# Kernel optimization log

Measured on AMD Instinct MI355X. Metric: run time of the kernel, lower is better.

The kernel has to match this reference:

```python
import jax, jax.numpy as jnp
import numpy as np

B, S, D, H = 2, 2048, 1024, 16
DH = D // H  # 64
SCALE = DH ** -0.5


def setup_inputs() -> dict:
    key = jax.random.key(0)
    ks = jax.random.split(key, 6)
    std = D ** -0.5
    return {
        "Q": jax.random.normal(ks[0], (B, S, D), jnp.float32),
        "prev": jax.random.normal(ks[1], (B, H, S, S), jnp.float32),
        "W_qkv": jax.random.normal(ks[2], (D, 3 * D), jnp.float32) * std,
        "b_qkv": jax.random.normal(ks[3], (3 * D,), jnp.float32) * 0.01,
        "W_out": jax.random.normal(ks[4], (D, D), jnp.float32) * std,
        "b_out": jax.random.normal(ks[5], (D,), jnp.float32) * 0.01,
    }


def reference(Q, prev, W_qkv, b_qkv, W_out, b_out):
    # fused QKV projection: [B,S,3D]
    qkv = jnp.einsum("bsd,de->bse", Q, W_qkv) + b_qkv
    # [B,S,H,3*DH] then split into q,k,v each [B,S,H,DH]
    qkv = qkv.reshape(B, S, H, 3 * DH)
    q, k, v = jnp.split(qkv, 3, axis=-1)
    # scores [B,H,S,S] with residual attention add
    scores = jnp.einsum("bqhd,bkhd->bhqk", q, k) * SCALE + prev
    attn = jax.nn.softmax(scores, axis=-1)  # dropout p=0.0 -> identity
    # context [B,S,H,DH] -> [B,S,D]
    context = jnp.einsum("bhqk,bkhd->bqhd", attn, v).reshape(B, S, D)
    output = jnp.einsum("bsd,de->bse", context, W_out) + b_out
    return output, scores
```

## Files before the change

kernel.cpp:

```cpp
#include <hip/hip_runtime.h>

typedef __attribute__((ext_vector_type(8))) short bf16x8;
typedef __attribute__((ext_vector_type(4))) float f32x4;
typedef __attribute__((ext_vector_type(4))) unsigned short u16x4;
typedef unsigned short ushort_t;
typedef unsigned int uint32;

constexpr int B_ = 2, S_ = 2048, D_ = 1024, H_ = 16, DH_ = 64;
constexpr int M_TOK = B_ * S_;
constexpr int N_QKV = 3 * D_;

#define DEV __device__ __forceinline__

DEV ushort_t f2bf(float f) {
  uint32 u = __builtin_bit_cast(uint32, f);
  u += 0x7fffu + ((u >> 16) & 1u);
  return (ushort_t)(u >> 16);
}

DEV void gll16(const void* g, void* l) {
  __builtin_amdgcn_global_load_lds(
      (const __attribute__((address_space(1))) void*)g,
      (__attribute__((address_space(3))) void*)l, 16, 0, 0);
}

__global__ __launch_bounds__(256) void k_cvt_q(const float* __restrict__ in,
                                               ushort_t* __restrict__ out) {
  int i = (blockIdx.x * 256 + threadIdx.x) * 4;
  float4 v = *(const float4*)(in + i);
  u16x4 o;
  o.x = f2bf(v.x); o.y = f2bf(v.y); o.z = f2bf(v.z); o.w = f2bf(v.w);
  *(u16x4*)(out + i) = o;
}

__global__ __launch_bounds__(256) void k_transpose_cvt(const float* __restrict__ in,
                                                       ushort_t* __restrict__ out,
                                                       int R, int C) {
  __shared__ float t[32][33];
  int bx = blockIdx.x, by = blockIdx.y;
  int tx = threadIdx.x & 31, ty = threadIdx.x >> 5;
#pragma unroll
  for (int i = 0; i < 4; ++i) {
    int r = by * 32 + ty + i * 8;
    t[ty + i * 8][tx] = in[(size_t)r * C + bx * 32 + tx];
  }
  __syncthreads();
#pragma unroll
  for (int i = 0; i < 4; ++i) {
    int orow = bx * 32 + ty + i * 8;
    int ocol = by * 32 + tx;
    out[(size_t)orow * R + ocol] = f2bf(t[tx][ty + i * 8]);
  }
}

__global__ __launch_bounds__(256) void k_gemm_qkv(
    const ushort_t* __restrict__ A,
    const ushort_t* __restrict__ Bt,
    const float* __restrict__ bias,
    ushort_t* __restrict__ qh,
    ushort_t* __restrict__ kh,
    ushort_t* __restrict__ vT) {
  constexpr int K = 1024;
  __shared__ ushort_t lA[128 * 32];
  __shared__ ushort_t lB[128 * 32];
  const int t = threadIdx.x, lane = t & 63, w = t >> 6;
  const int wm = w >> 1, wn = w & 1;
  const int bm = blockIdx.x & 31, bn = blockIdx.x >> 5;

  f32x4 acc[4][4];
#pragma unroll
  for (int i = 0; i < 4; ++i)
#pragma unroll
    for (int j = 0; j < 4; ++j) acc[i][j] = f32x4{0.f, 0.f, 0.f, 0.f};

  const int srow = t >> 2;
  const int scol = (t & 3) * 8;
  for (int k0 = 0; k0 < K; k0 += 32) {
    __syncthreads();
    gll16(A + (size_t)(bm * 128 + srow) * K + k0 + scol, lA + srow * 32 + scol);
    gll16(A + (size_t)(bm * 128 + 64 + srow) * K + k0 + scol, lA + (64 + srow) * 32 + scol);
    gll16(Bt + (size_t)(bn * 128 + srow) * K + k0 + scol, lB + srow * 32 + scol);
    gll16(Bt + (size_t)(bn * 128 + 64 + srow) * K + k0 + scol, lB + (64 + srow) * 32 + scol);
    asm volatile("s_waitcnt vmcnt(0)" ::: "memory");
    __syncthreads();
    bf16x8 af[4], bfr[4];
#pragma unroll
    for (int i = 0; i < 4; ++i)
      af[i] = *(const bf16x8*)(lA + (wm * 64 + i * 16 + (lane & 15)) * 32 + (lane >> 4) * 8);
#pragma unroll
    for (int j = 0; j < 4; ++j)
      bfr[j] = *(const bf16x8*)(lB + (wn * 64 + j * 16 + (lane & 15)) * 32 + (lane >> 4) * 8);
#pragma unroll
    for (int i = 0; i < 4; ++i)
#pragma unroll
      for (int j = 0; j < 4; ++j)
        acc[i][j] = __builtin_amdgcn_mfma_f32_16x16x32_bf16(af[i], bfr[j], acc[i][j], 0, 0, 0);
  }
#pragma unroll
  for (int i = 0; i < 4; ++i) {
#pragma unroll
    for (int j = 0; j < 4; ++j) {
#pragma unroll
      for (int p = 0; p < 4; ++p) {
        int row = bm * 128 + wm * 64 + i * 16 + (lane >> 4) * 4 + p;
        int col = bn * 128 + wn * 64 + j * 16 + (lane & 15);
        float v = acc[i][j][p] + bias[col];
        ushort_t bv = f2bf(v);
        int b = row >> 11, s = row & (S_ - 1);
        int h = col / 192, r = col - h * 192;
        size_t bh = (size_t)(b * H_ + h);
        if (r < 64)
          qh[(bh * S_ + s) * 64 + r] = bv;
        else if (r < 128)
          kh[(bh * S_ + s) * 64 + (r - 64)] = bv;
        else
          vT[(bh * 64 + (r - 128)) * S_ + s] = bv;
      }
    }
  }
}

__global__ __launch_bounds__(256, 2) void k_scores_pipe(
    const ushort_t* __restrict__ qhp,
    const ushort_t* __restrict__ khp,
    const float* __restrict__ prev,
    float* __restrict__ scores,
    float* __restrict__ pstats) {
  __shared__ ushort_t lK[512 * 64];
  const int t = threadIdx.x, lane = t & 63, w = t >> 6;
  int idx = (int)blockIdx.x;
  idx = (idx & 7) * 512 + (idx >> 3);
  const int rt = idx & 31, ct = (idx >> 5) & 3, bh = idx >> 7;
  const int row0 = rt * 64 + w * 16;
  const int kt0 = ct * 512;
  const int lo = lane & 15, hi = lane >> 4;

  const ushort_t* qb = qhp + ((size_t)bh * S_ + row0) * 64;
  const ushort_t* kb = khp + ((size_t)bh * S_ + kt0) * 64;
  const float* pb = prev + (size_t)bh * S_ * S_ + (size_t)(row0 + lo) * S_ + kt0;
  float* sb = scores + (size_t)bh * S_ * S_ + (size_t)(row0 + lo) * S_ + kt0;

  bf16x8 qf0 = *(const bf16x8*)(qb + lo * 64 + hi * 8);
  bf16x8 qf1 = *(const bf16x8*)(qb + lo * 64 + 32 + hi * 8);

#pragma unroll
  for (int i = 0; i < 16; ++i) {
    int u = i * 256 + t;
    int r = u >> 3;
    int s = (u & 7) * 16;
    int cb = s ^ ((r & 7) << 4);
    gll16(kb + (size_t)r * 64 + cb / 2, (ushort_t*)lK + u * 8);
  }
  float4 pcur[8];
#pragma unroll
  for (int kf = 0; kf < 8; ++kf)
    pcur[kf] = *(const float4*)(pb + kf * 16 + hi * 4);
  asm volatile("s_waitcnt vmcnt(0)" ::: "memory");
  __syncthreads();

  const int swz = (lo & 7) << 4;
  const char* lkb = (const char*)lK;

  for (int c = 0; c < 4; ++c) {
    float4 pnext[8];
    if (c < 3) {
#pragma unroll
      for (int kf = 0; kf < 8; ++kf)
        pnext[kf] = *(const float4*)(pb + (c + 1) * 128 + kf * 16 + hi * 4);
    }
    f32x4 acc[8];
#pragma unroll
    for (int kf = 0; kf < 8; ++kf) acc[kf] = f32x4{0.f, 0.f, 0.f, 0.f};
#pragma unroll
    for (int kf = 0; kf < 8; ++kf) {
      int krow = c * 128 + kf * 16 + lo;
      bf16x8 k0 = *(const bf16x8*)(lkb + krow * 128 + ((hi * 16) ^ swz));
      bf16x8 k1 = *(const bf16x8*)(lkb + krow * 128 + ((64 + hi * 16) ^ swz));
      acc[kf] = __builtin_amdgcn_mfma_f32_16x16x32_bf16(k0, qf0, acc[kf], 0, 0, 0);
      acc[kf] = __builtin_amdgcn_mfma_f32_16x16x32_bf16(k1, qf1, acc[kf], 0, 0, 0);
    }
    float tmax = -1e30f;
#pragma unroll
    for (int kf = 0; kf < 8; ++kf) {
      acc[kf][0] = acc[kf][0] * 0.125f + pcur[kf].x;
      acc[kf][1] = acc[kf][1] * 0.125f + pcur[kf].y;
      acc[kf][2] = acc[kf][2] * 0.125f + pcur[kf].z;
      acc[kf][3] = acc[kf][3] * 0.125f + pcur[kf].w;
      *(float4*)(sb + c * 128 + kf * 16 + hi * 4) =
          float4{acc[kf][0], acc[kf][1], acc[kf][2], acc[kf][3]};
      tmax = fmaxf(tmax, fmaxf(fmaxf(acc[kf][0], acc[kf][1]), fmaxf(acc[kf][2], acc[kf][3])));
    }
    tmax = fmaxf(tmax, __shfl_xor(tmax, 16));
    tmax = fmaxf(tmax, __shfl_xor(tmax, 32));
    float lsum = 0.f;
#pragma unroll
    for (int kf = 0; kf < 8; ++kf) {
      float e0 = __expf(acc[kf][0] - tmax);
      float e1 = __expf(acc[kf][1] - tmax);
      float e2 = __expf(acc[kf][2] - tmax);
      float e3 = __expf(acc[kf][3] - tmax);
      lsum += (e0 + e1) + (e2 + e3);
    }
    lsum += __shfl_xor(lsum, 16);
    lsum += __shfl_xor(lsum, 32);
    if (hi == 0)
      *(float2*)(pstats + (((size_t)bh * S_ + row0 + lo) * 16 + ct * 4 + c) * 2) =
          float2{tmax, lsum};
    if (c < 3) {
#pragma unroll
      for (int kf = 0; kf < 8; ++kf) pcur[kf] = pnext[kf];
    }
  }
}

__global__ __launch_bounds__(256, 4) void k_pv(
    const float* __restrict__ scores,
    const float* __restrict__ pstats,
    const ushort_t* __restrict__ vT,
    ushort_t* __restrict__ ctx) {
  const int t = threadIdx.x, lane = t & 63, w = t >> 6;
  const int idx = (int)gridDim.x - 1 - (int)blockIdx.x;
  const int bh = idx >> 5, rt = idx & 31;
  const int row0 = rt * 64 + w * 16;
  const int lo = lane & 15, hi = lane >> 4;

  const float* sb = scores + (size_t)bh * S_ * S_ + (size_t)(row0 + lo) * S_;
  const ushort_t* vb = vT + (size_t)bh * 64 * S_;

  const float* ps = pstats + ((size_t)bh * S_ + row0 + lo) * 32;
  float2 pp[16];
#pragma unroll
  for (int i = 0; i < 16; ++i) pp[i] = *(const float2*)(ps + i * 2);
  float m = pp[0].x;
#pragma unroll
  for (int i = 1; i < 16; ++i) m = fmaxf(m, pp[i].x);
  float l = 0.f;
#pragma unroll
  for (int i = 0; i < 16; ++i) l += pp[i].y * __expf(pp[i].x - m);
  const float c = m + __logf(l);

  f32x4 acco[4];
#pragma unroll
  for (int dn = 0; dn < 4; ++dn) acco[dn] = f32x4{0.f, 0.f, 0.f, 0.f};

  float4 scur[8];
#pragma unroll
  for (int kc = 0; kc < 4; ++kc) {
    scur[kc * 2]     = *(const float4*)(sb + kc * 32 + hi * 8);
    scur[kc * 2 + 1] = *(const float4*)(sb + kc * 32 + hi * 8 + 4);
  }

  for (int it = 0; it < 16; ++it) {
    const int kt = it * 128;
    bf16x8 vf[4][4];
#pragma unroll
    for (int kc = 0; kc < 4; ++kc)
#pragma unroll
      for (int dn = 0; dn < 4; ++dn)
        vf[kc][dn] = *(const bf16x8*)(vb + (size_t)(dn * 16 + lo) * S_ + kt + kc * 32 + hi * 8);
    float4 snext[8];
    if (it < 15) {
#pragma unroll
      for (int kc = 0; kc < 4; ++kc) {
        snext[kc * 2]     = *(const float4*)(sb + kt + 128 + kc * 32 + hi * 8);
        snext[kc * 2 + 1] = *(const float4*)(sb + kt + 128 + kc * 32 + hi * 8 + 4);
      }
    }
#pragma unroll
    for (int kc = 0; kc < 4; ++kc) {
      float4 s0 = scur[kc * 2], s1 = scur[kc * 2 + 1];
      bf16x8 pa;
      pa[0] = (short)f2bf(__expf(s0.x - c));
      pa[1] = (short)f2bf(__expf(s0.y - c));
      pa[2] = (short)f2bf(__expf(s0.z - c));
      pa[3] = (short)f2bf(__expf(s0.w - c));
      pa[4] = (short)f2bf(__expf(s1.x - c));
      pa[5] = (short)f2bf(__expf(s1.y - c));
      pa[6] = (short)f2bf(__expf(s1.z - c));
      pa[7] = (short)f2bf(__expf(s1.w - c));
#pragma unroll
      for (int dn = 0; dn < 4; ++dn)
        acco[dn] = __builtin_amdgcn_mfma_f32_16x16x32_bf16(vf[kc][dn], pa, acco[dn], 0, 0, 0);
    }
    if (it < 15) {
#pragma unroll
      for (int kf = 0; kf < 8; ++kf) scur[kf] = snext[kf];
    }
  }
  const int b = bh >> 4, h = bh & 15;
#pragma unroll
  for (int dn = 0; dn < 4; ++dn) {
    u16x4 ov;
#pragma unroll
    for (int p = 0; p < 4; ++p) ov[p] = f2bf(acco[dn][p]);
    *(u16x4*)(ctx + (size_t)(b * S_ + row0 + lo) * D_ + h * 64 + dn * 16 + hi * 4) = ov;
  }
}

__global__ __launch_bounds__(256) void k_gemm_out(
    const ushort_t* __restrict__ A,
    const ushort_t* __restrict__ Bt,
    const float* __restrict__ bias,
    float* __restrict__ out) {
  constexpr int K = 1024;
  __shared__ ushort_t lA[128 * 32];
  __shared__ ushort_t lB[128 * 32];
  const int t = threadIdx.x, lane = t & 63, w = t >> 6;
  const int wm = w >> 1, wn = w & 1;
  const int bm = blockIdx.x & 31, bn = blockIdx.x >> 5;

  f32x4 acc[4][4];
#pragma unroll
  for (int i = 0; i < 4; ++i)
#pragma unroll
    for (int j = 0; j < 4; ++j) acc[i][j] = f32x4{0.f, 0.f, 0.f, 0.f};

  const int srow = t >> 2;
  const int scol = (t & 3) * 8;
  for (int k0 = 0; k0 < K; k0 += 32) {
    __syncthreads();
    gll16(A + (size_t)(bm * 128 + srow) * K + k0 + scol, lA + srow * 32 + scol);
    gll16(A + (size_t)(bm * 128 + 64 + srow) * K + k0 + scol, lA + (64 + srow) * 32 + scol);
    gll16(Bt + (size_t)(bn * 128 + srow) * K + k0 + scol, lB + srow * 32 + scol);
    gll16(Bt + (size_t)(bn * 128 + 64 + srow) * K + k0 + scol, lB + (64 + srow) * 32 + scol);
    asm volatile("s_waitcnt vmcnt(0)" ::: "memory");
    __syncthreads();
    bf16x8 af[4], bfr[4];
#pragma unroll
    for (int i = 0; i < 4; ++i)
      af[i] = *(const bf16x8*)(lA + (wm * 64 + i * 16 + (lane & 15)) * 32 + (lane >> 4) * 8);
#pragma unroll
    for (int j = 0; j < 4; ++j)
      bfr[j] = *(const bf16x8*)(lB + (wn * 64 + j * 16 + (lane & 15)) * 32 + (lane >> 4) * 8);
#pragma unroll
    for (int i = 0; i < 4; ++i)
#pragma unroll
      for (int j = 0; j < 4; ++j)
        acc[i][j] = __builtin_amdgcn_mfma_f32_16x16x32_bf16(af[i], bfr[j], acc[i][j], 0, 0, 0);
  }
#pragma unroll
  for (int i = 0; i < 4; ++i) {
#pragma unroll
    for (int j = 0; j < 4; ++j) {
#pragma unroll
      for (int p = 0; p < 4; ++p) {
        int row = bm * 128 + wm * 64 + i * 16 + (lane >> 4) * 4 + p;
        int col = bn * 128 + wn * 64 + j * 16 + (lane & 15);
        out[(size_t)row * 1024 + col] = acc[i][j][p] + bias[col];
      }
    }
  }
}

extern "C" void kernel_launch(void* const* d_in, const int* in_sizes, int n_in,
                              void* d_out, int out_size, void* d_ws, size_t ws_size,
                              hipStream_t stream) {
  (void)in_sizes; (void)n_in; (void)out_size; (void)ws_size;
  const float* Q     = (const float*)d_in[0];
  const float* prev  = (const float*)d_in[1];
  const float* W_qkv = (const float*)d_in[2];
  const float* b_qkv = (const float*)d_in[3];
  const float* W_out = (const float*)d_in[4];
  const float* b_out = (const float*)d_in[5];
  float* out = (float*)d_out;
  float* scores_out = out + (size_t)M_TOK * D_;

  char* ws = (char*)d_ws;
  ushort_t* Qb    = (ushort_t*)(ws + (size_t)0);
  ushort_t* WqkvT = (ushort_t*)(ws + ((size_t)8  << 20));
  ushort_t* WoutT = (ushort_t*)(ws + ((size_t)14 << 20));
  ushort_t* qh    = (ushort_t*)(ws + ((size_t)16 << 20));
  ushort_t* kh    = (ushort_t*)(ws + ((size_t)24 << 20));
  ushort_t* vT    = (ushort_t*)(ws + ((size_t)32 << 20));
  ushort_t* ctx   = (ushort_t*)(ws + ((size_t)40 << 20));
  float*    pstats = (float*)Qb;

  k_cvt_q<<<4096, 256, 0, stream>>>(Q, Qb);
  k_transpose_cvt<<<dim3(96, 32), 256, 0, stream>>>(W_qkv, WqkvT, 1024, 3072);
  k_transpose_cvt<<<dim3(32, 32), 256, 0, stream>>>(W_out, WoutT, 1024, 1024);
  k_gemm_qkv<<<768, 256, 0, stream>>>(Qb, WqkvT, b_qkv, qh, kh, vT);
  k_scores_pipe<<<4096, 256, 0, stream>>>(qh, kh, prev, scores_out, pstats);
  k_pv<<<1024, 256, 0, stream>>>(scores_out, pstats, vT, ctx);
  k_gemm_out<<<256, 256, 0, stream>>>(ctx, WoutT, b_out, out);
}
```

Before: 485.9 us.

## Halve scores tile width for occupancy and double-buffer score prefetch in PV

The scores kernel now handles 256 key columns per block instead of 512. This halves LDS use, lets four blocks share a CU, and doubles the grid, with block order remapped so column tiles stay adjacent. The PV kernel replaces its single prefetch buffer with two register buffers that alternate. Score loads are issued two steps ahead, and the exponentials are computed before the V loads, to hide more memory latency. This costs more registers, so its launch bound drops to three blocks per CU.

```diff
diff --git a/kernel.cpp b/kernel.cpp
--- a/kernel.cpp
+++ b/kernel.cpp
@@ -120,19 +120,19 @@
   }
 }
 
-__global__ __launch_bounds__(256, 2) void k_scores_pipe(
+__global__ __launch_bounds__(256, 4) void k_scores_pipe(
     const ushort_t* __restrict__ qhp,
     const ushort_t* __restrict__ khp,
     const float* __restrict__ prev,
     float* __restrict__ scores,
     float* __restrict__ pstats) {
-  __shared__ ushort_t lK[512 * 64];
+  __shared__ ushort_t lK[256 * 64];
   const int t = threadIdx.x, lane = t & 63, w = t >> 6;
   int idx = (int)blockIdx.x;
-  idx = (idx & 7) * 512 + (idx >> 3);
-  const int rt = idx & 31, ct = (idx >> 5) & 3, bh = idx >> 7;
+  idx = (idx & 7) * 1024 + (idx >> 3);
+  const int ct = idx & 7, rt = (idx >> 3) & 31, bh = idx >> 8;
   const int row0 = rt * 64 + w * 16;
-  const int kt0 = ct * 512;
+  const int kt0 = ct * 256;
   const int lo = lane & 15, hi = lane >> 4;
 
   const ushort_t* qb = qhp + ((size_t)bh * S_ + row0) * 64;
@@ -144,7 +144,7 @@
   bf16x8 qf1 = *(const bf16x8*)(qb + lo * 64 + 32 + hi * 8);
 
 #pragma unroll
-  for (int i = 0; i < 16; ++i) {
+  for (int i = 0; i < 8; ++i) {
     int u = i * 256 + t;
     int r = u >> 3;
     int s = (u & 7) * 16;
@@ -161,12 +161,13 @@
   const int swz = (lo & 7) << 4;
   const char* lkb = (const char*)lK;
 
-  for (int c = 0; c < 4; ++c) {
+#pragma unroll
+  for (int c = 0; c < 2; ++c) {
     float4 pnext[8];
-    if (c < 3) {
+    if (c < 1) {
 #pragma unroll
       for (int kf = 0; kf < 8; ++kf)
-        pnext[kf] = *(const float4*)(pb + (c + 1) * 128 + kf * 16 + hi * 4);
+        pnext[kf] = *(const float4*)(pb + 128 + kf * 16 + hi * 4);
     }
     f32x4 acc[8];
 #pragma unroll
@@ -204,16 +205,16 @@
     lsum += __shfl_xor(lsum, 16);
     lsum += __shfl_xor(lsum, 32);
     if (hi == 0)
-      *(float2*)(pstats + (((size_t)bh * S_ + row0 + lo) * 16 + ct * 4 + c) * 2) =
+      *(float2*)(pstats + (((size_t)bh * S_ + row0 + lo) * 16 + ct * 2 + c) * 2) =
           float2{tmax, lsum};
-    if (c < 3) {
+    if (c < 1) {
 #pragma unroll
       for (int kf = 0; kf < 8; ++kf) pcur[kf] = pnext[kf];
     }
   }
 }
 
-__global__ __launch_bounds__(256, 4) void k_pv(
+__global__ __launch_bounds__(256, 3) void k_pv(
     const float* __restrict__ scores,
     const float* __restrict__ pstats,
     const ushort_t* __restrict__ vT,
@@ -243,50 +244,58 @@
 #pragma unroll
   for (int dn = 0; dn < 4; ++dn) acco[dn] = f32x4{0.f, 0.f, 0.f, 0.f};
 
-  float4 scur[8];
+  float4 sA[8], sB[8];
 #pragma unroll
   for (int kc = 0; kc < 4; ++kc) {
-    scur[kc * 2]     = *(const float4*)(sb + kc * 32 + hi * 8);
-    scur[kc * 2 + 1] = *(const float4*)(sb + kc * 32 + hi * 8 + 4);
-  }
-
-  for (int it = 0; it < 16; ++it) {
-    const int kt = it * 128;
-    bf16x8 vf[4][4];
-#pragma unroll
-    for (int kc = 0; kc < 4; ++kc)
-#pragma unroll
-      for (int dn = 0; dn < 4; ++dn)
-        vf[kc][dn] = *(const bf16x8*)(vb + (size_t)(dn * 16 + lo) * S_ + kt + kc * 32 + hi * 8);
-    float4 snext[8];
-    if (it < 15) {
-#pragma unroll
-      for (int kc = 0; kc < 4; ++kc) {
-        snext[kc * 2]     = *(const float4*)(sb + kt + 128 + kc * 32 + hi * 8);
-        snext[kc * 2 + 1] = *(const float4*)(sb + kt + 128 + kc * 32 + hi * 8 + 4);
-      }
-    }
-#pragma unroll
-    for (int kc = 0; kc < 4; ++kc) {
-      float4 s0 = scur[kc * 2], s1 = scur[kc * 2 + 1];
-      bf16x8 pa;
-      pa[0] = (short)f2bf(__expf(s0.x - c));
-      pa[1] = (short)f2bf(__expf(s0.y - c));
-      pa[2] = (short)f2bf(__expf(s0.z - c));
-      pa[3] = (short)f2bf(__expf(s0.w - c));
-      pa[4] = (short)f2bf(__expf(s1.x - c));
-      pa[5] = (short)f2bf(__expf(s1.y - c));
-      pa[6] = (short)f2bf(__expf(s1.z - c));
-      pa[7] = (short)f2bf(__expf(s1.w - c));
-#pragma unroll
-      for (int dn = 0; dn < 4; ++dn)
-        acco[dn] = __builtin_amdgcn_mfma_f32_16x16x32_bf16(vf[kc][dn], pa, acco[dn], 0, 0, 0);
-    }
-    if (it < 15) {
-#pragma unroll
-      for (int kf = 0; kf < 8; ++kf) scur[kf] = snext[kf];
-    }
-  }
+    sA[kc * 2]     = *(const float4*)(sb + kc * 32 + hi * 8);
+    sA[kc * 2 + 1] = *(const float4*)(sb + kc * 32 + hi * 8 + 4);
+  }
+#pragma unroll
+  for (int kc = 0; kc < 4; ++kc) {
+    sB[kc * 2]     = *(const float4*)(sb + 128 + kc * 32 + hi * 8);
+    sB[kc * 2 + 1] = *(const float4*)(sb + 128 + kc * 32 + hi * 8 + 4);
+  }
+
+#define PV_STEP(SBUF, IT)                                                     \
+  {                                                                           \
+    const int kt = (IT) * 128;                                                \
+    bf16x8 pa[4];                                                             \
+    _Pragma("unroll") for (int kc = 0; kc < 4; ++kc) {                        \
+      float4 s0 = SBUF[kc * 2], s1 = SBUF[kc * 2 + 1];                        \
+      pa[kc][0] = (short)f2bf(__expf(s0.x - c));                              \
+      pa[kc][1] = (short)f2bf(__expf(s0.y - c));                              \
+      pa[kc][2] = (short)f2bf(__expf(s0.z - c));                              \
+      pa[kc][3] = (short)f2bf(__expf(s0.w - c));                              \
+      pa[kc][4] = (short)f2bf(__expf(s1.x - c));                              \
+      pa[kc][5] = (short)f2bf(__expf(s1.y - c));                              \
+      pa[kc][6] = (short)f2bf(__expf(s1.z - c));                              \
+      pa[kc][7] = (short)f2bf(__expf(s1.w - c));                              \
+    }                                                                         \
+    bf16x8 vf[4][4];                                                          \
+    _Pragma("unroll") for (int kc = 0; kc < 4; ++kc)                          \
+        _Pragma("unroll") for (int dn = 0; dn < 4; ++dn)                      \
+            vf[kc][dn] = *(const bf16x8*)(vb + (size_t)(dn * 16 + lo) * S_ +  \
+                                          kt + kc * 32 + hi * 8);             \
+    if ((IT) < 14) {                                                          \
+      _Pragma("unroll") for (int kc = 0; kc < 4; ++kc) {                      \
+        SBUF[kc * 2] = *(const float4*)(sb + kt + 256 + kc * 32 + hi * 8);    \
+        SBUF[kc * 2 + 1] =                                                    \
+            *(const float4*)(sb + kt + 256 + kc * 32 + hi * 8 + 4);           \
+      }                                                                       \
+    }                                                                         \
+    _Pragma("unroll") for (int kc = 0; kc < 4; ++kc)                          \
+        _Pragma("unroll") for (int dn = 0; dn < 4; ++dn)                      \
+            acco[dn] = __builtin_amdgcn_mfma_f32_16x16x32_bf16(               \
+                vf[kc][dn], pa[kc], acco[dn], 0, 0, 0);                       \
+  }
+
+#pragma unroll
+  for (int it2 = 0; it2 < 8; ++it2) {
+    PV_STEP(sA, it2 * 2);
+    PV_STEP(sB, it2 * 2 + 1);
+  }
+#undef PV_STEP
+
   const int b = bh >> 4, h = bh & 15;
 #pragma unroll
   for (int dn = 0; dn < 4; ++dn) {
@@ -379,7 +388,7 @@
   k_transpose_cvt<<<dim3(96, 32), 256, 0, stream>>>(W_qkv, WqkvT, 1024, 3072);
   k_transpose_cvt<<<dim3(32, 32), 256, 0, stream>>>(W_out, WoutT, 1024, 1024);
   k_gemm_qkv<<<768, 256, 0, stream>>>(Qb, WqkvT, b_qkv, qh, kh, vT);
-  k_scores_pipe<<<4096, 256, 0, stream>>>(qh, kh, prev, scores_out, pstats);
+  k_scores_pipe<<<8192, 256, 0, stream>>>(qh, kh, prev, scores_out, pstats);
   k_pv<<<1024, 256, 0, stream>>>(scores_out, pstats, vT, ctx);
   k_gemm_out<<<256, 256, 0, stream>>>(ctx, WoutT, b_out, out);
 }
```

After: 510.1 us. 1.05x slower.

## Fuse PV into scores kernel with online softmax and split-K combine

Applied to the files above, without the earlier changes.

Folds the P·V product into the scores kernel. Each block keeps a running max and sum across its four 128-column chunks, stages bf16 probabilities in LDS, and accumulates partial outputs with MFMA. A new small kernel merges the four column-split partials using the per-split stats. This removes the second full read of the 128 MB fp32 scores tensor by k_pv, at the cost of extra LDS, more register pressure in the scores kernel, and bf16 rounding of the partial outputs.

```diff
diff --git a/kernel.cpp b/kernel.cpp
--- a/kernel.cpp
+++ b/kernel.cpp
@@ -16,6 +16,11 @@
   uint32 u = __builtin_bit_cast(uint32, f);
   u += 0x7fffu + ((u >> 16) & 1u);
   return (ushort_t)(u >> 16);
+}
+
+DEV float bf2f(ushort_t u) {
+  uint32 x = ((uint32)u) << 16;
+  return __builtin_bit_cast(float, x);
 }
 
 DEV void gll16(const void* g, void* l) {
@@ -120,13 +125,16 @@
   }
 }
 
-__global__ __launch_bounds__(256, 2) void k_scores_pipe(
+__global__ __launch_bounds__(256, 2) void k_scores_pv(
     const ushort_t* __restrict__ qhp,
     const ushort_t* __restrict__ khp,
+    const ushort_t* __restrict__ vT,
     const float* __restrict__ prev,
     float* __restrict__ scores,
-    float* __restrict__ pstats) {
+    float* __restrict__ pstats,
+    ushort_t* __restrict__ Opart) {
   __shared__ ushort_t lK[512 * 64];
+  __shared__ ushort_t Plds[4][2048];
   const int t = threadIdx.x, lane = t & 63, w = t >> 6;
   int idx = (int)blockIdx.x;
   idx = (idx & 7) * 512 + (idx >> 3);
@@ -137,6 +145,7 @@
 
   const ushort_t* qb = qhp + ((size_t)bh * S_ + row0) * 64;
   const ushort_t* kb = khp + ((size_t)bh * S_ + kt0) * 64;
+  const ushort_t* vb = vT + (size_t)bh * 64 * S_ + kt0;
   const float* pb = prev + (size_t)bh * S_ * S_ + (size_t)(row0 + lo) * S_ + kt0;
   float* sb = scores + (size_t)bh * S_ * S_ + (size_t)(row0 + lo) * S_ + kt0;
 
@@ -160,8 +169,21 @@
 
   const int swz = (lo & 7) << 4;
   const char* lkb = (const char*)lK;
+  char* pw = (char*)&Plds[w][0];
+
+  f32x4 acco[4];
+#pragma unroll
+  for (int dn = 0; dn < 4; ++dn) acco[dn] = f32x4{0.f, 0.f, 0.f, 0.f};
+  float m_run = -1e30f, l_run = 0.f;
 
   for (int c = 0; c < 4; ++c) {
+    bf16x8 vf[4][4];
+#pragma unroll
+    for (int kc = 0; kc < 4; ++kc)
+#pragma unroll
+      for (int dn = 0; dn < 4; ++dn)
+        vf[kc][dn] = *(const bf16x8*)(vb + (size_t)(dn * 16 + lo) * S_ +
+                                      c * 128 + kc * 32 + hi * 8);
     float4 pnext[8];
     if (c < 3) {
 #pragma unroll
@@ -192,108 +214,98 @@
     }
     tmax = fmaxf(tmax, __shfl_xor(tmax, 16));
     tmax = fmaxf(tmax, __shfl_xor(tmax, 32));
+    float m_new = fmaxf(m_run, tmax);
+    float fs = __expf(m_run - m_new);
     float lsum = 0.f;
 #pragma unroll
     for (int kf = 0; kf < 8; ++kf) {
-      float e0 = __expf(acc[kf][0] - tmax);
-      float e1 = __expf(acc[kf][1] - tmax);
-      float e2 = __expf(acc[kf][2] - tmax);
-      float e3 = __expf(acc[kf][3] - tmax);
+      float e0 = __expf(acc[kf][0] - m_new);
+      float e1 = __expf(acc[kf][1] - m_new);
+      float e2 = __expf(acc[kf][2] - m_new);
+      float e3 = __expf(acc[kf][3] - m_new);
       lsum += (e0 + e1) + (e2 + e3);
+      u16x4 pk;
+      pk.x = f2bf(e0); pk.y = f2bf(e1); pk.z = f2bf(e2); pk.w = f2bf(e3);
+      int byte = (lo * 256 + kf * 32 + hi * 8) ^ swz;
+      *(u16x4*)(pw + byte) = pk;
     }
     lsum += __shfl_xor(lsum, 16);
     lsum += __shfl_xor(lsum, 32);
-    if (hi == 0)
-      *(float2*)(pstats + (((size_t)bh * S_ + row0 + lo) * 16 + ct * 4 + c) * 2) =
-          float2{tmax, lsum};
-    if (c < 3) {
-#pragma unroll
-      for (int kf = 0; kf < 8; ++kf) pcur[kf] = pnext[kf];
-    }
-  }
-}
-
-__global__ __launch_bounds__(256, 4) void k_pv(
-    const float* __restrict__ scores,
-    const float* __restrict__ pstats,
-    const ushort_t* __restrict__ vT,
-    ushort_t* __restrict__ ctx) {
-  const int t = threadIdx.x, lane = t & 63, w = t >> 6;
-  const int idx = (int)gridDim.x - 1 - (int)blockIdx.x;
-  const int bh = idx >> 5, rt = idx & 31;
-  const int row0 = rt * 64 + w * 16;
-  const int lo = lane & 15, hi = lane >> 4;
-
-  const float* sb = scores + (size_t)bh * S_ * S_ + (size_t)(row0 + lo) * S_;
-  const ushort_t* vb = vT + (size_t)bh * 64 * S_;
-
-  const float* ps = pstats + ((size_t)bh * S_ + row0 + lo) * 32;
-  float2 pp[16];
-#pragma unroll
-  for (int i = 0; i < 16; ++i) pp[i] = *(const float2*)(ps + i * 2);
-  float m = pp[0].x;
-#pragma unroll
-  for (int i = 1; i < 16; ++i) m = fmaxf(m, pp[i].x);
-  float l = 0.f;
-#pragma unroll
-  for (int i = 0; i < 16; ++i) l += pp[i].y * __expf(pp[i].x - m);
-  const float c = m + __logf(l);
-
-  f32x4 acco[4];
-#pragma unroll
-  for (int dn = 0; dn < 4; ++dn) acco[dn] = f32x4{0.f, 0.f, 0.f, 0.f};
-
-  float4 scur[8];
-#pragma unroll
-  for (int kc = 0; kc < 4; ++kc) {
-    scur[kc * 2]     = *(const float4*)(sb + kc * 32 + hi * 8);
-    scur[kc * 2 + 1] = *(const float4*)(sb + kc * 32 + hi * 8 + 4);
-  }
-
-  for (int it = 0; it < 16; ++it) {
-    const int kt = it * 128;
-    bf16x8 vf[4][4];
-#pragma unroll
-    for (int kc = 0; kc < 4; ++kc)
-#pragma unroll
-      for (int dn = 0; dn < 4; ++dn)
-        vf[kc][dn] = *(const bf16x8*)(vb + (size_t)(dn * 16 + lo) * S_ + kt + kc * 32 + hi * 8);
-    float4 snext[8];
-    if (it < 15) {
-#pragma unroll
-      for (int kc = 0; kc < 4; ++kc) {
-        snext[kc * 2]     = *(const float4*)(sb + kt + 128 + kc * 32 + hi * 8);
-        snext[kc * 2 + 1] = *(const float4*)(sb + kt + 128 + kc * 32 + hi * 8 + 4);
-      }
-    }
+    m_run = m_new;
+    l_run = l_run * fs + lsum;
+#pragma unroll
+    for (int dn = 0; dn < 4; ++dn)
+#pragma unroll
+      for (int p = 0; p < 4; ++p) acco[dn][p] *= fs;
 #pragma unroll
     for (int kc = 0; kc < 4; ++kc) {
-      float4 s0 = scur[kc * 2], s1 = scur[kc * 2 + 1];
-      bf16x8 pa;
-      pa[0] = (short)f2bf(__expf(s0.x - c));
-      pa[1] = (short)f2bf(__expf(s0.y - c));
-      pa[2] = (short)f2bf(__expf(s0.z - c));
-      pa[3] = (short)f2bf(__expf(s0.w - c));
-      pa[4] = (short)f2bf(__expf(s1.x - c));
-      pa[5] = (short)f2bf(__expf(s1.y - c));
-      pa[6] = (short)f2bf(__expf(s1.z - c));
-      pa[7] = (short)f2bf(__expf(s1.w - c));
+      int byte = (lo * 256 + kc * 64 + hi * 16) ^ swz;
+      bf16x8 pa = *(const bf16x8*)(pw + byte);
 #pragma unroll
       for (int dn = 0; dn < 4; ++dn)
         acco[dn] = __builtin_amdgcn_mfma_f32_16x16x32_bf16(vf[kc][dn], pa, acco[dn], 0, 0, 0);
     }
-    if (it < 15) {
-#pragma unroll
-      for (int kf = 0; kf < 8; ++kf) scur[kf] = snext[kf];
-    }
-  }
-  const int b = bh >> 4, h = bh & 15;
+    if (c < 3) {
+#pragma unroll
+      for (int kf = 0; kf < 8; ++kf) pcur[kf] = pnext[kf];
+    }
+  }
+  ushort_t* ob = Opart + (((size_t)bh * S_ + row0 + lo) * 4 + ct) * 64;
 #pragma unroll
   for (int dn = 0; dn < 4; ++dn) {
     u16x4 ov;
 #pragma unroll
     for (int p = 0; p < 4; ++p) ov[p] = f2bf(acco[dn][p]);
-    *(u16x4*)(ctx + (size_t)(b * S_ + row0 + lo) * D_ + h * 64 + dn * 16 + hi * 4) = ov;
+    *(u16x4*)(ob + dn * 16 + hi * 4) = ov;
+  }
+  if (hi == 0)
+    *(float2*)(pstats + (((size_t)bh * S_ + row0 + lo) * 4 + ct) * 2) =
+        float2{m_run, l_run};
+}
+
+__global__ __launch_bounds__(256) void k_combine(
+    const float* __restrict__ pstats,
+    const ushort_t* __restrict__ Opart,
+    ushort_t* __restrict__ ctx) {
+  const int t = threadIdx.x;
+  const int row = blockIdx.x * 64 + (t >> 2);
+  const int hi4 = t & 3;
+  const int bh = row >> 11, s = row & (S_ - 1);
+
+  const float* ps = pstats + (size_t)row * 8;
+  float2 st[4];
+#pragma unroll
+  for (int i = 0; i < 4; ++i) st[i] = *(const float2*)(ps + i * 2);
+  float m = fmaxf(fmaxf(st[0].x, st[1].x), fmaxf(st[2].x, st[3].x));
+  float den = 0.f;
+#pragma unroll
+  for (int i = 0; i < 4; ++i) den += st[i].y * __expf(st[i].x - m);
+  float sc[4];
+#pragma unroll
+  for (int i = 0; i < 4; ++i) sc[i] = __expf(st[i].x - m) / den;
+
+  const ushort_t* ob = Opart + (size_t)row * 256 + hi4 * 16;
+  float o[16];
+#pragma unroll
+  for (int j = 0; j < 16; ++j) o[j] = 0.f;
+#pragma unroll
+  for (int i = 0; i < 4; ++i) {
+    bf16x8 a0 = *(const bf16x8*)(ob + i * 64);
+    bf16x8 a1 = *(const bf16x8*)(ob + i * 64 + 8);
+#pragma unroll
+    for (int j = 0; j < 8; ++j) {
+      o[j]     += bf2f((ushort_t)a0[j]) * sc[i];
+      o[8 + j] += bf2f((ushort_t)a1[j]) * sc[i];
+    }
+  }
+  const int b = bh >> 4, h = bh & 15;
+  ushort_t* cp = ctx + (size_t)(b * S_ + s) * D_ + h * 64 + hi4 * 16;
+#pragma unroll
+  for (int g = 0; g < 4; ++g) {
+    u16x4 ov;
+#pragma unroll
+    for (int p = 0; p < 4; ++p) ov[p] = f2bf(o[g * 4 + p]);
+    *(u16x4*)(cp + g * 4) = ov;
   }
 }
 
@@ -373,13 +385,14 @@
   ushort_t* kh    = (ushort_t*)(ws + ((size_t)24 << 20));
   ushort_t* vT    = (ushort_t*)(ws + ((size_t)32 << 20));
   ushort_t* ctx   = (ushort_t*)(ws + ((size_t)40 << 20));
+  ushort_t* Opart = (ushort_t*)(ws + ((size_t)48 << 20));
   float*    pstats = (float*)Qb;
 
   k_cvt_q<<<4096, 256, 0, stream>>>(Q, Qb);
   k_transpose_cvt<<<dim3(96, 32), 256, 0, stream>>>(W_qkv, WqkvT, 1024, 3072);
   k_transpose_cvt<<<dim3(32, 32), 256, 0, stream>>>(W_out, WoutT, 1024, 1024);
   k_gemm_qkv<<<768, 256, 0, stream>>>(Qb, WqkvT, b_qkv, qh, kh, vT);
-  k_scores_pipe<<<4096, 256, 0, stream>>>(qh, kh, prev, scores_out, pstats);
-  k_pv<<<1024, 256, 0, stream>>>(scores_out, pstats, vT, ctx);
+  k_scores_pv<<<4096, 256, 0, stream>>>(qh, kh, vT, prev, scores_out, pstats, Opart);
+  k_combine<<<1024, 256, 0, stream>>>(pstats, Opart, ctx);
   k_gemm_out<<<256, 256, 0, stream>>>(ctx, WoutT, b_out, out);
 }
```

New measurement: 414.7 us, median of 2. 14.6% less time.
